# Optimization experiments

Hardware: AMD Instinct MI355X
Metric: run time of the kernel (lower is better)

## Reference

```python
import jax, jax.numpy as jnp
import numpy as np

GRAPH_ALPHA = 3.0
HOP_ALPHA = 0.05
TOP_K = 30


def conv1x1(x, W, b):
    # x: [B,C,N,T], W: [O,C] -> [B,O,N,T]
    return jnp.einsum('bcnt,oc->bont', x, W) + b[None, :, None, None]


def tconv(x, W, b):
    # temporal conv along T, kernel (1,3), 'same' padding. W: [O,I,1,3]
    y = jax.lax.conv_general_dilated(x, W, (1, 1), ((0, 0), (1, 1)),
                                     dimension_numbers=('NCHW', 'OIHW', 'NCHW'))
    return y + b[None, :, None, None]


def mixprop(x, adj, W, b):
    # 1-hop mix-prop graph diffusion (gcn_depth=1, hopalpha=0.05)
    n = adj.shape[0]
    A = adj + jnp.eye(n, dtype=adj.dtype)
    A = A / A.sum(axis=1, keepdims=True)
    h = HOP_ALPHA * x + (1.0 - HOP_ALPHA) * jnp.einsum('bcvt,vw->bcwt', x, A)
    return conv1x1(jnp.concatenate([x, h], axis=1), W, b)


def st_block(x, adj, tf_w, tf_b, tg_w, tg_b, g1_w, g1_b, g2_w, g2_b,
             end_w, end_b, out_w, out_b):
    h = jnp.tanh(tconv(x, tf_w, tf_b)) * jax.nn.sigmoid(tconv(x, tg_w, tg_b))
    h = mixprop(h, adj, g1_w, g1_b) + mixprop(h, adj.T, g2_w, g2_b)
    h = jax.nn.relu(conv1x1(h, end_w, end_b))
    return conv1x1(h, out_w, out_b)


def build_adj(idx, emb1, emb2, l1_w, l1_b, l2_w, l2_b):
    e1, e2 = emb1[idx], emb2[idx]
    n1 = jnp.tanh(GRAPH_ALPHA * (e1 @ l1_w.T + l1_b))
    n2 = jnp.tanh(GRAPH_ALPHA * (e2 @ l2_w.T + l2_b))
    a = n1 @ n2.T - n2 @ n1.T
    adj = jax.nn.relu(jnp.tanh(GRAPH_ALPHA * a))
    _, top_idx = jax.lax.top_k(adj, TOP_K)
    rows = jnp.arange(adj.shape[0])[:, None]
    mask = jnp.zeros_like(adj).at[rows, top_idx].set(1.0)
    return adj * mask


def setup_inputs() -> dict:
    B, T, N, D = 16, 128, 1024, 64
    ks = jax.random.split(jax.random.key(0), 24)
    def w(i, shape):
        return jax.random.normal(ks[i], shape, dtype=jnp.float32) * 0.1
    z = lambda *s: jnp.zeros(s, jnp.float32)
    return {
        'x': jax.random.normal(ks[0], (B, T, N), dtype=jnp.float32),
        'idx': jnp.arange(N, dtype=jnp.int32),
        'emb1': w(1, (N, D)), 'emb2': w(2, (N, D)),
        'lin1_w': w(3, (D, D)), 'lin1_b': z(D),
        'lin2_w': w(4, (D, D)), 'lin2_b': z(D),
        'w_start': w(5, (16, 1)), 'b_start': z(16),
        'enc_tf_w': w(6, (16, 16, 1, 3)), 'enc_tf_b': z(16),
        'enc_tg_w': w(7, (16, 16, 1, 3)), 'enc_tg_b': z(16),
        'enc_g1_w': w(8, (16, 32)), 'enc_g1_b': z(16),
        'enc_g2_w': w(9, (16, 32)), 'enc_g2_b': z(16),
        'enc_end_w': w(10, (32, 16)), 'enc_end_b': z(32),
        'enc_out_w': w(11, (64, 32)), 'enc_out_b': z(64),
        'dec_tf_w': w(12, (64, 64, 1, 3)), 'dec_tf_b': z(64),
        'dec_tg_w': w(13, (64, 64, 1, 3)), 'dec_tg_b': z(64),
        'dec_g1_w': w(14, (64, 128)), 'dec_g1_b': z(64),
        'dec_g2_w': w(15, (64, 128)), 'dec_g2_b': z(64),
        'dec_end_w': w(16, (32, 64)), 'dec_end_b': z(32),
        'dec_out_w': w(17, (16, 32)), 'dec_out_b': z(16),
        'w_end': w(18, (1, 16)), 'b_end': z(1),
    }


def reference(x, idx, emb1, emb2, lin1_w, lin1_b, lin2_w, lin2_b,
              w_start, b_start,
              enc_tf_w, enc_tf_b, enc_tg_w, enc_tg_b, enc_g1_w, enc_g1_b,
              enc_g2_w, enc_g2_b, enc_end_w, enc_end_b, enc_out_w, enc_out_b,
              dec_tf_w, dec_tf_b, dec_tg_w, dec_tg_b, dec_g1_w, dec_g1_b,
              dec_g2_w, dec_g2_b, dec_end_w, dec_end_b, dec_out_w, dec_out_b,
              w_end, b_end):
    adj = build_adj(idx, emb1, emb2, lin1_w, lin1_b, lin2_w, lin2_b)
    h = jnp.transpose(x, (0, 2, 1))[:, None]  # [B,1,N,T]
    h = conv1x1(h, w_start, b_start)          # [B,16,N,T]
    z = st_block(h, adj, enc_tf_w, enc_tf_b, enc_tg_w, enc_tg_b,
                 enc_g1_w, enc_g1_b, enc_g2_w, enc_g2_b,
                 enc_end_w, enc_end_b, enc_out_w, enc_out_b)  # [B,64,N,T]
    y = st_block(z, adj, dec_tf_w, dec_tf_b, dec_tg_w, dec_tg_b,
                 dec_g1_w, dec_g1_b, dec_g2_w, dec_g2_b,
                 dec_end_w, dec_end_b, dec_out_w, dec_out_b)  # [B,16,N,T]
    y = conv1x1(y, w_end, b_end)               # [B,1,N,T]
    return jnp.transpose(y[:, 0], (0, 2, 1))   # [B,T,N]
```

## Files before the change

### kernel.cpp

```cpp
#include <hip/hip_runtime.h>
#include <math.h>

#define NN   1024
#define TTL  128
#define NTP  131072
#define TOPK 30

#define OEGTF_T 0
#define OEGTF_C 48
#define OEGTF_B 96
#define OEGTG_T 112
#define OEGTG_C 160
#define OEGTG_B 208
#define OEE0    224
#define OEE1    736
#define OEE2    1248
#define OEEB    1760
#define OEOUT_W 1792
#define OEOUT_B 3840
#define ODTF_B  16192
#define ODTG_B  28544
#define ODEB    34752
#define OWC     34784
#define OBC     34816
#define ODEALL  59456
#define ODTW2   65600
#define OCF     77888
#define OCG     78080
#define WTOT    78272


__global__ void k_prep_weights(
    const float* __restrict__ w_start, const float* __restrict__ b_start,
    const float* __restrict__ etf_w, const float* __restrict__ etf_b,
    const float* __restrict__ etg_w, const float* __restrict__ etg_b,
    const float* __restrict__ eg1_w, const float* __restrict__ eg1_b,
    const float* __restrict__ eg2_w, const float* __restrict__ eg2_b,
    const float* __restrict__ eend_w, const float* __restrict__ eend_b,
    const float* __restrict__ eout_w, const float* __restrict__ eout_b,
    const float* __restrict__ dtf_w, const float* __restrict__ dtf_b,
    const float* __restrict__ dtg_w, const float* __restrict__ dtg_b,
    const float* __restrict__ dg1_w, const float* __restrict__ dg1_b,
    const float* __restrict__ dg2_w, const float* __restrict__ dg2_b,
    const float* __restrict__ dend_w, const float* __restrict__ dend_b,
    const float* __restrict__ dout_w, const float* __restrict__ dout_b,
    const float* __restrict__ w_end, const float* __restrict__ b_end,
    float* __restrict__ W)
{
    int tid = blockIdx.x*blockDim.x + threadIdx.x;
    int nthr = gridDim.x*blockDim.x;
    for (int id=tid; id<96; id+=nthr){
        int which = id/48; int r = id%48; int o = r/3, k = r%3;
        const float* w = which ? etg_w : etf_w;
        double t=0.0, c=0.0;
        for (int i=0;i<16;i++){
            double wv = (double)w[(o*16+i)*3+k];
            t += wv*(double)w_start[i];
            c += wv*(double)b_start[i];
        }
        W[(which?OEGTG_T:OEGTF_T)+o*3+k] = (float)t;
        W[(which?OEGTG_C:OEGTF_C)+o*3+k] = (float)c;
    }
    for (int i=tid;i<16;i+=nthr){
        W[OEGTF_B+i] = etf_b[i];
        W[OEGTG_B+i] = etg_b[i];
    }
    for (int id=tid; id<512; id+=nthr){
        int i = id>>5, o2 = id&31;
        double s0=0.0, s1=0.0, s2=0.0;
        for (int o=0;o<16;o++){
            double m0 = (double)eg1_w[o*32+i] + (double)eg2_w[o*32+i]
                      + 0.05*((double)eg1_w[o*32+16+i] + (double)eg2_w[o*32+16+i]);
            double m1 = 0.95*(double)eg1_w[o*32+16+i];
            double m2 = 0.95*(double)eg2_w[o*32+16+i];
            double ew = (double)eend_w[o2*16+o];
            s0 += ew*m0; s1 += ew*m1; s2 += ew*m2;
        }
        W[OEE0+i*32+o2]=(float)s0; W[OEE1+i*32+o2]=(float)s1; W[OEE2+i*32+o2]=(float)s2;
    }
    for (int o2=tid; o2<32; o2+=nthr){
        double s = (double)eend_b[o2];
        for (int o=0;o<16;o++) s += (double)eend_w[o2*16+o]*((double)eg1_b[o]+(double)eg2_b[o]);
        W[OEEB+o2] = (float)s;
    }
    for (int i=tid;i<64;i+=nthr){
        W[ODTF_B+i]=dtf_b[i]; W[ODTG_B+i]=dtg_b[i];
    }
    for (int id=tid; id<12288; id+=nthr){
        int oc = id/3072; int rem = id%3072; int j = rem/96; int q = rem%96;
        const float* w = (q<48) ? dtf_w : dtg_w;
        int q2 = (q<48) ? q : q-48;
        int o = q2/3, k = q2%3;
        double s = 0.0;
        for (int i=0;i<64;i++)
            s += (double)w[((oc*16+o)*64+i)*3+k]*(double)eout_w[i*32+j];
        W[ODTW2+id] = (float)s;
    }
    for (int id=tid; id<384; id+=nthr){
        int which = id/192; int r = id%192;
        int oc = r/48; int q = r%48; int o = q/3, k = q%3;
        const float* w = which ? dtg_w : dtf_w;
        double s = 0.0;
        for (int i=0;i<64;i++)
            s += (double)w[((oc*16+o)*64+i)*3+k]*(double)eout_b[i];
        W[(which?OCG:OCF) + oc*48 + o*3 + k] = (float)s;
    }
    for (int id=tid; id<6144; id+=nthr){
        int i = id/96, j = id%96;
        double s = 0.0;
        if (j < 32){
            int o2 = j;
            for (int o=0;o<64;o++){
                double m1 = 0.95*(double)dg1_w[o*128+64+i];
                s += (double)dend_w[o2*64+o]*m1;
            }
        } else if (j < 64){
            int o2 = j-32;
            for (int o=0;o<64;o++){
                double m2 = 0.95*(double)dg2_w[o*128+64+i];
                s += (double)dend_w[o2*64+o]*m2;
            }
        } else {
            int o2 = j-64;
            for (int o=0;o<64;o++){
                double m0 = (double)dg1_w[o*128+i] + (double)dg2_w[o*128+i]
                          + 0.05*((double)dg1_w[o*128+64+i] + (double)dg2_w[o*128+64+i]);
                s += (double)dend_w[o2*64+o]*m0;
            }
        }
        W[ODEALL+id] = (float)s;
    }
    for (int o2=tid; o2<32; o2+=nthr){
        double s = (double)dend_b[o2];
        for (int o=0;o<64;o++) s += (double)dend_w[o2*64+o]*((double)dg1_b[o]+(double)dg2_b[o]);
        W[ODEB+o2] = (float)s;
        double wc = 0.0;
        for (int o3=0;o3<16;o3++) wc += (double)w_end[o3]*(double)dout_w[o3*32+o2];
        W[OWC+o2] = (float)wc;
    }
    if (tid==0){
        double bc = (double)b_end[0];
        for (int o3=0;o3<16;o3++) bc += (double)w_end[o3]*(double)dout_b[o3];
        W[OBC] = (float)bc;
    }
}

__global__ void k_emb(const int* __restrict__ idxp,
                      const float* __restrict__ emb1, const float* __restrict__ emb2,
                      const float* __restrict__ l1w, const float* __restrict__ l1b,
                      const float* __restrict__ l2w, const float* __restrict__ l2b,
                      double* __restrict__ n1, double* __restrict__ n2)
{
    int id = blockIdx.x*blockDim.x + threadIdx.x;
    int i = id>>6, d = id&63;
    int ii = idxp[i];
    double a1 = (double)l1b[d], a2 = (double)l2b[d];
    for (int k=0;k<64;k++){
        a1 += (double)emb1[ii*64+k]*(double)l1w[d*64+k];
        a2 += (double)emb2[ii*64+k]*(double)l2w[d*64+k];
    }
    n1[id] = tanh(3.0*a1);
    n2[id] = tanh(3.0*a2);
}

__global__ __launch_bounds__(64) void k_topk(
    const double* __restrict__ n1, const double* __restrict__ n2,
    int* __restrict__ topc, double* __restrict__ topv,
    double* __restrict__ rs1, double* __restrict__ colsum)
{
    __shared__ double arow[NN];
    __shared__ double sn1[64], sn2[64];
    int i = blockIdx.x, lane = threadIdx.x;
    sn1[lane] = n1[i*64+lane];
    sn2[lane] = n2[i*64+lane];
    __syncthreads();
    for (int jb=0;jb<16;jb++){
        int j = jb*64 + lane;
        const double* p2 = n2 + j*64;
        const double* p1 = n1 + j*64;
        double d1v=0.0, d2v=0.0;
        for (int d=0;d<64;d++){ d1v += sn1[d]*p2[d]; d2v += sn2[d]*p1[d]; }
        double a = tanh(3.0*(d1v - d2v));
        arow[j] = a>0.0 ? a : 0.0;
    }
    __syncthreads();
    double rsum = 0.0;
    for (int r=0;r<TOPK;r++){
        double bv = -2.0; int bj = 1<<30;
        for (int jb=0;jb<16;jb++){
            int j = jb*64+lane;
            double v = arow[j];
            if (v>bv || (v==bv && j<bj)){ bv=v; bj=j; }
        }
        for (int off=32; off>=1; off>>=1){
            double ov = __shfl_xor(bv, off, 64);
            int    oj = __shfl_xor(bj, off, 64);
            if (ov>bv || (ov==bv && oj<bj)){ bv=ov; bj=oj; }
        }
        if (lane == (bj & 63)) arow[bj] = -2.0;
        if (lane == 0){
            topc[i*TOPK+r] = bj;
            topv[i*TOPK+r] = bv;
            if (bv > 0.0) atomicAdd(&colsum[bj], bv);
        }
        rsum += (bv > 0.0 ? bv : 0.0);
        __syncthreads();
    }
    if (lane == 0) rs1[i] = 1.0 + rsum;
}

__global__ void k_csc(const int* __restrict__ topc, const double* __restrict__ topv,
                      const double* __restrict__ rs1,
                      int* __restrict__ ccount, int* __restrict__ cidx, float* __restrict__ cw)
{
    int w = blockIdx.x*blockDim.x + threadIdx.x;
    if (w >= NN) return;
    double rv = rs1[w];
    for (int r=0;r<TOPK;r++){
        double v = topv[w*TOPK+r];
        if (v > 0.0){
            int col = topc[w*TOPK+r];
            int pos = atomicAdd(&ccount[col], 1);
            cidx[(long)col*NN+pos] = w;
            cw  [(long)col*NN+pos] = (float)(v / rv);
        }
    }
}

__global__ void k_pad(int* __restrict__ ccount, int* __restrict__ cidx, float* __restrict__ cw)
{
    int col = blockIdx.x*blockDim.x + threadIdx.x;
    if (col >= NN) return;
    int cnt = ccount[col];
    int padded = (cnt + 7) & ~7;
    for (int e = cnt; e < padded; e++){
        cidx[(long)col*NN + e] = 0;
        cw  [(long)col*NN + e] = 0.0f;
    }
    ccount[col] = padded;
}

__global__ void k_post1(const double* __restrict__ colsum, const double* __restrict__ rs1,
                        double* __restrict__ rs2, float* __restrict__ d1, float* __restrict__ d2)
{
    int v = blockIdx.x*blockDim.x + threadIdx.x;
    if (v >= NN) return;
    double r2 = 1.0 + colsum[v];
    rs2[v] = r2;
    d2[v] = (float)(1.0/r2);
    d1[v] = (float)(1.0/rs1[v]);
}

__global__ void k_post2(const int* __restrict__ topc, const double* __restrict__ topv,
                        const double* __restrict__ rs2, float* __restrict__ ew2)
{
    int e = blockIdx.x*blockDim.x + threadIdx.x;
    if (e >= NN*TOPK) return;
    double v = topv[e];
    ew2[e] = (v > 0.0) ? (float)(v / rs2[topc[e]]) : 0.0f;
}

__global__ __launch_bounds__(256) void k_xT(const float* __restrict__ x, float* __restrict__ xT)
{
    __shared__ float tile[32][33];
    int b = blockIdx.z, t0 = blockIdx.x*32, n0 = blockIdx.y*32;
    int tx = threadIdx.x, ty = threadIdx.y;
    const float* xb = x + (long)b*NTP;
    for (int r=0;r<4;r++){
        int tl = ty + 8*r;
        tile[tl][tx] = xb[(long)(t0+tl)*NN + n0 + tx];
    }
    __syncthreads();
    float* ob = xT + (long)b*NTP;
    for (int r=0;r<4;r++){
        int nl = ty + 8*r;
        ob[(long)(n0+nl)*TTL + t0 + tx] = tile[tx][nl];
    }
}


__global__ __launch_bounds__(256) void k_enc_gg(const float* __restrict__ xT,
    float* __restrict__ eg, float* __restrict__ es1, float* __restrict__ es2,
    const float* __restrict__ Wt,
    const int* __restrict__ ccount, const int* __restrict__ cidx, const float* __restrict__ cw,
    const int* __restrict__ topc, const float* __restrict__ ew2,
    const float* __restrict__ d1, const float* __restrict__ d2,
    long S, int b0)
{
    __shared__ float ldsg[NN*6];
    int tid = threadIdx.x, c = blockIdx.y, cb = blockIdx.z, t0 = blockIdx.x*4;
    float ft[3], fc[3], gt[3], gcc[3];
    #pragma unroll
    for (int k=0;k<3;k++){
        ft[k]=Wt[OEGTF_T+c*3+k]; fc[k]=Wt[OEGTF_C+c*3+k];
        gt[k]=Wt[OEGTG_T+c*3+k]; gcc[k]=Wt[OEGTG_C+c*3+k];
    }
    float fb = Wt[OEGTF_B+c], gb = Wt[OEGTG_B+c];
    const float* xb = xT + (long)(b0+cb)*NTP;
    long base = (long)c*S + (long)cb*NTP;
    for (int k=0;k<16;k++){
        int idx = k*256 + tid;
        int v = idx>>2, tl = idx&3, t = t0+tl;
        const float* xp = xb + (long)v*TTL + t;
        float xc = xp[0];
        float atf = fb + ft[1]*xc + fc[1];
        float atg = gb + gt[1]*xc + gcc[1];
        if (t>0){ float xl = xp[-1]; atf += ft[0]*xl + fc[0]; atg += gt[0]*xl + gcc[0]; }
        if (t<TTL-1){ float xr = xp[1]; atf += ft[2]*xr + fc[2]; atg += gt[2]*xr + gcc[2]; }
        float gv = tanhf(atf)/(1.0f+expf(-atg));
        ldsg[v*6+tl] = gv;
        eg[base + (long)v*TTL + t] = gv;
    }
    __syncthreads();
    for (int wb=0;wb<4;wb++){
        int w = wb*256 + tid;
        const float* gw = &ldsg[w*6];
        float g0=gw[0], g1=gw[1], g2=gw[2], g3=gw[3];
        long p = base + (long)w*TTL + t0;
        float dv = d1[w];
        float a0=g0*dv, a1=g1*dv, a2=g2*dv, a3=g3*dv;
        int cnt = ccount[w];
        const int* ci = cidx + (long)w*NN;
        const float* cv = cw + (long)w*NN;
        for (int e0=0; e0<cnt; e0+=8){
            #pragma unroll
            for (int k=0;k<8;k++){
                float wt_ = cv[e0+k];
                const float* s = &ldsg[ci[e0+k]*6];
                a0 += wt_*s[0]; a1 += wt_*s[1]; a2 += wt_*s[2]; a3 += wt_*s[3];
            }
        }
        es1[p]=a0; es1[p+1]=a1; es1[p+2]=a2; es1[p+3]=a3;
        float d2v = d2[w];
        a0=g0*d2v; a1=g1*d2v; a2=g2*d2v; a3=g3*d2v;
        const int* tc = topc + w*TOPK;
        const float* e2 = ew2 + w*TOPK;
        for (int r0=0;r0<TOPK;r0+=6){
            #pragma unroll
            for (int k=0;k<6;k++){
                float wv = e2[r0+k];
                const float* s = &ldsg[tc[r0+k]*6];
                a0 += wv*s[0]; a1 += wv*s[1]; a2 += wv*s[2]; a3 += wv*s[3];
            }
        }
        es2[p]=a0; es2[p+1]=a1; es2[p+2]=a2; es2[p+3]=a3;
    }
}

__global__ __launch_bounds__(256) void k_enc_tail(const float* __restrict__ Bp,
    float* __restrict__ E32, const float* __restrict__ Wt, long S)
{
    long p = (long)blockIdx.x*256 + threadIdx.x;
    float e[32];
    #pragma unroll
    for (int o2=0;o2<32;o2++) e[o2] = Wt[OEEB+o2];
    for (int i=0;i<16;i++){
        float a = Bp[(long)i*S+p], b = Bp[(long)(16+i)*S+p], c = Bp[(long)(32+i)*S+p];
        const float* w0 = Wt+OEE0+i*32;
        const float* w1 = Wt+OEE1+i*32;
        const float* w2 = Wt+OEE2+i*32;
        #pragma unroll
        for (int o2=0;o2<32;o2++) e[o2] += w0[o2]*a + w1[o2]*b + w2[o2]*c;
    }
    #pragma unroll
    for (int o2=0;o2<32;o2++){
        float v = e[o2];
        E32[(long)o2*S+p] = v>0.0f ? v : 0.0f;
    }
}

__global__ __launch_bounds__(256) void k_dec_gate(const float* __restrict__ E32,
    float* __restrict__ g, const float* __restrict__ Wt, long S)
{
    int bx = blockIdx.x;
    int oc = (bx >> 3) & 3;
    long vpair = (long)(bx >> 5)*8 + (bx & 7);
    int tid = threadIdx.x;
    int t = tid & 127, vv = tid >> 7;
    long vstrip = vpair*2 + vv;
    long pos = vstrip*TTL + t;
    bool hasL = (t>0), hasR = (t<TTL-1);
    float af[16], ag[16];
    #pragma unroll
    for (int o=0;o<16;o++){
        float bf = Wt[ODTF_B+oc*16+o] + Wt[OCF+oc*48+o*3+1];
        float bg = Wt[ODTG_B+oc*16+o] + Wt[OCG+oc*48+o*3+1];
        if (hasL){ bf += Wt[OCF+oc*48+o*3];   bg += Wt[OCG+oc*48+o*3]; }
        if (hasR){ bf += Wt[OCF+oc*48+o*3+2]; bg += Wt[OCG+oc*48+o*3+2]; }
        af[o]=bf; ag[o]=bg;
    }
    #pragma unroll 1
    for (int j=0;j<32;j++){
        const float* xp = E32 + (long)j*S + pos;
        float xc = xp[0];
        float xl = hasL ? xp[-1] : 0.0f;
        float xr = hasR ? xp[1]  : 0.0f;
        const float* wfg = Wt + ODTW2 + (long)(oc*32+j)*96;
        #pragma unroll
        for (int o=0;o<16;o++){
            af[o] += wfg[o*3]*xl + wfg[o*3+1]*xc + wfg[o*3+2]*xr;
            ag[o] += wfg[48+o*3]*xl + wfg[48+o*3+1]*xc + wfg[48+o*3+2]*xr;
        }
    }
    #pragma unroll
    for (int o=0;o<16;o++){
        g[(long)(oc*16+o)*S + pos] = tanhf(af[o])/(1.0f+expf(-ag[o]));
    }
}

__global__ __launch_bounds__(256) void k_dec_conv(const float* __restrict__ g,
    float* __restrict__ Cp, float* __restrict__ P0p,
    const float* __restrict__ Wt, long S)
{
    long p = (long)blockIdx.x*256 + threadIdx.x;
    int jc = blockIdx.y;
    if (jc == 0){
        float a1[32], a2[32];
        #pragma unroll
        for (int jj=0;jj<32;jj++){ a1[jj]=0.0f; a2[jj]=0.0f; }
        #pragma unroll 1
        for (int i=0;i<64;i++){
            float gv = g[(long)i*S+p];
            const float* wr = Wt + ODEALL + i*96;
            #pragma unroll
            for (int jj=0;jj<32;jj++){ a1[jj] += wr[jj]*gv; a2[jj] += wr[32+jj]*gv; }
        }
        #pragma unroll
        for (int jj=0;jj<32;jj++){
            Cp[(long)jj*S+p] = a1[jj];
            Cp[(long)(32+jj)*S+p] = a2[jj];
        }
    } else {
        float a0[32];
        #pragma unroll
        for (int jj=0;jj<32;jj++) a0[jj] = Wt[ODEB+jj];
        #pragma unroll 1
        for (int i=0;i<64;i++){
            float gv = g[(long)i*S+p];
            const float* wr = Wt + ODEALL + i*96 + 64;
            #pragma unroll
            for (int jj=0;jj<32;jj++) a0[jj] += wr[jj]*gv;
        }
        #pragma unroll
        for (int jj=0;jj<32;jj++) P0p[(long)jj*S+p] = a0[jj];
    }
}

__global__ __launch_bounds__(256) void k_graph32(const float* __restrict__ P1,
    const float* __restrict__ P2, float* __restrict__ Q12,
    const int* __restrict__ ccount, const int* __restrict__ cidx, const float* __restrict__ cw,
    const int* __restrict__ topc, const float* __restrict__ ew2,
    const float* __restrict__ d1, const float* __restrict__ d2, long S)
{
    __shared__ float lds[NN*6];
    int tid = threadIdx.x;
    int ch = blockIdx.y;
    int cb = blockIdx.z;
    long base = (long)ch*S + (long)cb*NTP;
    int t0 = blockIdx.x*4;
    float r0[4], r1[4], r2[4], r3[4];
    {
        const float* src = P1 + base;
        for (int k=0;k<16;k++){
            int idx = k*256 + tid;
            int v = idx>>2, tl = idx&3;
            lds[v*6+tl] = src[(long)v*TTL + t0 + tl];
        }
        __syncthreads();
        for (int wb=0;wb<4;wb++){
            int w = wb*256 + tid;
            const float* gw = &lds[w*6];
            float dv = d1[w];
            float a0=gw[0]*dv, a1=gw[1]*dv, a2=gw[2]*dv, a3=gw[3]*dv;
            int cnt = ccount[w];
            const int* ci = cidx + (long)w*NN;
            const float* cv = cw + (long)w*NN;
            for (int e0=0; e0<cnt; e0+=8){
                #pragma unroll
                for (int k=0;k<8;k++){
                    float wt_ = cv[e0+k];
                    const float* s = &lds[ci[e0+k]*6];
                    a0 += wt_*s[0]; a1 += wt_*s[1]; a2 += wt_*s[2]; a3 += wt_*s[3];
                }
            }
            r0[wb]=a0; r1[wb]=a1; r2[wb]=a2; r3[wb]=a3;
        }
    }
    __syncthreads();
    {
        const float* src = P2 + base;
        for (int k=0;k<16;k++){
            int idx = k*256 + tid;
            int v = idx>>2, tl = idx&3;
            lds[v*6+tl] = src[(long)v*TTL + t0 + tl];
        }
        __syncthreads();
        for (int wb=0;wb<4;wb++){
            int w = wb*256 + tid;
            const float* gw = &lds[w*6];
            float dv = d2[w];
            float a0=gw[0]*dv, a1=gw[1]*dv, a2=gw[2]*dv, a3=gw[3]*dv;
            const int* tc = topc + w*TOPK;
            const float* e2 = ew2 + w*TOPK;
            for (int q0=0;q0<TOPK;q0+=6){
                #pragma unroll
                for (int k=0;k<6;k++){
                    float wv = e2[q0+k];
                    const float* s = &lds[tc[q0+k]*6];
                    a0 += wv*s[0]; a1 += wv*s[1]; a2 += wv*s[2]; a3 += wv*s[3];
                }
            }
            long p = base + (long)w*TTL + t0;
            Q12[p]   = r0[wb] + a0;
            Q12[p+1] = r1[wb] + a1;
            Q12[p+2] = r2[wb] + a2;
            Q12[p+3] = r3[wb] + a3;
        }
    }
}

__global__ __launch_bounds__(256) void k_dec_tail(const float* __restrict__ P0,
    const float* __restrict__ Q12,
    const float* __restrict__ Wt, float* __restrict__ out, long S, int b0)
{
    long p = (long)blockIdx.x*256 + threadIdx.x;
    float res = Wt[OBC];
    #pragma unroll 8
    for (int o2=0;o2<32;o2++){
        float e = P0[(long)o2*S+p] + Q12[(long)o2*S+p];
        e = e>0.0f ? e : 0.0f;
        res += Wt[OWC+o2]*e;
    }
    int cb = (int)(p >> 17);
    long r = p & (NTP-1);
    int v = (int)(r >> 7), t = (int)(r & (TTL-1));
    out[((long)(b0+cb)*TTL + t)*NN + v] = res;
}


extern "C" void kernel_launch(void* const* d_in, const int* in_sizes, int n_in,
                              void* d_out, int out_size, void* d_ws, size_t ws_size,
                              hipStream_t stream)
{
    const float* x      = (const float*)d_in[0];
    const int*   idx    = (const int*)  d_in[1];
    const float* emb1   = (const float*)d_in[2];
    const float* emb2   = (const float*)d_in[3];
    const float* lin1_w = (const float*)d_in[4];
    const float* lin1_b = (const float*)d_in[5];
    const float* lin2_w = (const float*)d_in[6];
    const float* lin2_b = (const float*)d_in[7];
    const float* w_start= (const float*)d_in[8];
    const float* b_start= (const float*)d_in[9];
    const float* etf_w  = (const float*)d_in[10];
    const float* etf_b  = (const float*)d_in[11];
    const float* etg_w  = (const float*)d_in[12];
    const float* etg_b  = (const float*)d_in[13];
    const float* eg1_w  = (const float*)d_in[14];
    const float* eg1_b  = (const float*)d_in[15];
    const float* eg2_w  = (const float*)d_in[16];
    const float* eg2_b  = (const float*)d_in[17];
    const float* eend_w = (const float*)d_in[18];
    const float* eend_b = (const float*)d_in[19];
    const float* eout_w = (const float*)d_in[20];
    const float* eout_b = (const float*)d_in[21];
    const float* dtf_w  = (const float*)d_in[22];
    const float* dtf_b  = (const float*)d_in[23];
    const float* dtg_w  = (const float*)d_in[24];
    const float* dtg_b  = (const float*)d_in[25];
    const float* dg1_w  = (const float*)d_in[26];
    const float* dg1_b  = (const float*)d_in[27];
    const float* dg2_w  = (const float*)d_in[28];
    const float* dg2_b  = (const float*)d_in[29];
    const float* dend_w = (const float*)d_in[30];
    const float* dend_b = (const float*)d_in[31];
    const float* dout_w = (const float*)d_in[32];
    const float* dout_b = (const float*)d_in[33];
    const float* w_end  = (const float*)d_in[34];
    const float* b_end  = (const float*)d_in[35];
    float* out = (float*)d_out;

    char* basep = (char*)d_ws;
    size_t cur = 0;
    auto alloc = [&](size_t bytes)->void* {
        void* p = basep + cur;
        cur = (cur + bytes + 511) & ~(size_t)511;
        return p;
    };
    float*  W     = (float*) alloc(WTOT*sizeof(float));
    double* n1    = (double*)alloc(65536*sizeof(double));
    double* n2    = (double*)alloc(65536*sizeof(double));
    double* topv  = (double*)alloc((size_t)NN*TOPK*sizeof(double));
    int*    topc  = (int*)   alloc((size_t)NN*TOPK*sizeof(int));
    double* rs1   = (double*)alloc(NN*sizeof(double));
    double* rs2   = (double*)alloc(NN*sizeof(double));
    double* colsum= (double*)alloc(NN*sizeof(double));
    float*  d1a   = (float*) alloc(NN*sizeof(float));
    float*  d2a   = (float*) alloc(NN*sizeof(float));
    float*  ew2   = (float*) alloc((size_t)NN*TOPK*sizeof(float));
    int*    ccount= (int*)   alloc(NN*sizeof(int));
    int*    cidx  = (int*)   alloc((size_t)NN*NN*sizeof(int));
    float*  cw    = (float*) alloc((size_t)NN*NN*sizeof(float));
    float*  xT    = (float*) alloc((size_t)16*NTP*sizeof(float));

    size_t perb = (size_t)176 * NTP * sizeof(float);
    int CB = 1;
    for (int c = 16; c >= 1; c >>= 1){
        if (cur + perb*(size_t)c <= ws_size){ CB = c; break; }
    }
    long S = (long)CB * NTP;
    float* A = (float*)alloc((size_t)64*S*sizeof(float));
    float* B = (float*)alloc((size_t)48*S*sizeof(float));
    float* C = (float*)alloc((size_t)64*S*sizeof(float));

    (void)hipMemsetAsync(colsum, 0, NN*sizeof(double), stream);
    (void)hipMemsetAsync(ccount, 0, NN*sizeof(int), stream);

    k_prep_weights<<<32,256,0,stream>>>(
        w_start,b_start, etf_w,etf_b, etg_w,etg_b, eg1_w,eg1_b, eg2_w,eg2_b,
        eend_w,eend_b, eout_w,eout_b, dtf_w,dtf_b, dtg_w,dtg_b, dg1_w,dg1_b,
        dg2_w,dg2_b, dend_w,dend_b, dout_w,dout_b, w_end,b_end, W);
    k_emb<<<256,256,0,stream>>>(idx, emb1, emb2, lin1_w, lin1_b, lin2_w, lin2_b, n1, n2);
    k_topk<<<NN,64,0,stream>>>(n1, n2, topc, topv, rs1, colsum);
    k_csc<<<4,256,0,stream>>>(topc, topv, rs1, ccount, cidx, cw);
    k_pad<<<4,256,0,stream>>>(ccount, cidx, cw);
    k_post1<<<4,256,0,stream>>>(colsum, rs1, rs2, d1a, d2a);
    k_post2<<<(NN*TOPK+255)/256,256,0,stream>>>(topc, topv, rs2, ew2);
    k_xT<<<dim3(4,32,16),dim3(32,8),0,stream>>>(x, xT);

    int nch = 16 / CB;
    for (int ch=0; ch<nch; ch++){
        int b0 = ch*CB;
        k_enc_gg<<<dim3(32,16,CB),256,0,stream>>>(xT, B, B+(long)16*S, B+(long)32*S, W,
            ccount,cidx,cw, topc,ew2, d1a,d2a, S, b0);
        k_enc_tail<<<512*CB,256,0,stream>>>(B, A, W, S);
        k_dec_gate<<<2048*CB,256,0,stream>>>(A, C, W, S);
        k_dec_conv<<<dim3(512*CB,2),256,0,stream>>>(C, A, B, W, S);
        k_graph32<<<dim3(32,32,CB),256,0,stream>>>(A, A+(long)32*S, C,
            ccount,cidx,cw, topc,ew2, d1a,d2a, S);
        k_dec_tail<<<512*CB,256,0,stream>>>(B, C, W, out, S, b0);
    }
    (void)in_sizes; (void)n_in; (void)out_size;
}
```

Before: 4.369 ms.

## Switch intermediates to time-major layout and vectorize graph gathers with float4

Intermediate activations now use a [t][node] layout that matches the input x and the output. This removes the separate x transpose kernel and the transposed output store, and makes the graph kernels' LDS staging and global writes coalesced per node. Graph gathers now read packed float4 tiles and fetch CSC indices and weights as int4/float4. The top-k lists are padded to 32 entries so the second-hop loop can be fully vectorized. The decoder gate kernel's temporal neighbours are now NN elements apart, which changes its access pattern and grid shape.

```diff
diff --git a/kernel.cpp b/kernel.cpp
--- a/kernel.cpp
+++ b/kernel.cpp
@@ -252,42 +252,33 @@
 }
 
 __global__ void k_post2(const int* __restrict__ topc, const double* __restrict__ topv,
-                        const double* __restrict__ rs2, float* __restrict__ ew2)
+                        const double* __restrict__ rs2,
+                        int* __restrict__ topc2, float* __restrict__ ew2b)
 {
     int e = blockIdx.x*blockDim.x + threadIdx.x;
-    if (e >= NN*TOPK) return;
-    double v = topv[e];
-    ew2[e] = (v > 0.0) ? (float)(v / rs2[topc[e]]) : 0.0f;
-}
-
-__global__ __launch_bounds__(256) void k_xT(const float* __restrict__ x, float* __restrict__ xT)
-{
-    __shared__ float tile[32][33];
-    int b = blockIdx.z, t0 = blockIdx.x*32, n0 = blockIdx.y*32;
-    int tx = threadIdx.x, ty = threadIdx.y;
-    const float* xb = x + (long)b*NTP;
-    for (int r=0;r<4;r++){
-        int tl = ty + 8*r;
-        tile[tl][tx] = xb[(long)(t0+tl)*NN + n0 + tx];
-    }
-    __syncthreads();
-    float* ob = xT + (long)b*NTP;
-    for (int r=0;r<4;r++){
-        int nl = ty + 8*r;
-        ob[(long)(n0+nl)*TTL + t0 + tx] = tile[tx][nl];
-    }
-}
-
-
-__global__ __launch_bounds__(256) void k_enc_gg(const float* __restrict__ xT,
+    if (e >= NN*32) return;
+    int w = e>>5, r = e&31;
+    if (r < TOPK){
+        double v = topv[w*TOPK+r];
+        int c = topc[w*TOPK+r];
+        topc2[e] = (v > 0.0) ? c : 0;
+        ew2b[e]  = (v > 0.0) ? (float)(v / rs2[c]) : 0.0f;
+    } else {
+        topc2[e] = 0;
+        ew2b[e]  = 0.0f;
+    }
+}
+
+
+__global__ __launch_bounds__(256) void k_enc_gg(const float* __restrict__ x,
     float* __restrict__ eg, float* __restrict__ es1, float* __restrict__ es2,
     const float* __restrict__ Wt,
     const int* __restrict__ ccount, const int* __restrict__ cidx, const float* __restrict__ cw,
-    const int* __restrict__ topc, const float* __restrict__ ew2,
+    const int* __restrict__ topc2, const float* __restrict__ ew2b,
     const float* __restrict__ d1, const float* __restrict__ d2,
     long S, int b0)
 {
-    __shared__ float ldsg[NN*6];
+    __shared__ float4 lds4[NN];
     int tid = threadIdx.x, c = blockIdx.y, cb = blockIdx.z, t0 = blockIdx.x*4;
     float ft[3], fc[3], gt[3], gcc[3];
     #pragma unroll
@@ -296,54 +287,77 @@
         gt[k]=Wt[OEGTG_T+c*3+k]; gcc[k]=Wt[OEGTG_C+c*3+k];
     }
     float fb = Wt[OEGTF_B+c], gb = Wt[OEGTG_B+c];
-    const float* xb = xT + (long)(b0+cb)*NTP;
-    long base = (long)c*S + (long)cb*NTP;
-    for (int k=0;k<16;k++){
-        int idx = k*256 + tid;
-        int v = idx>>2, tl = idx&3, t = t0+tl;
-        const float* xp = xb + (long)v*TTL + t;
-        float xc = xp[0];
-        float atf = fb + ft[1]*xc + fc[1];
-        float atg = gb + gt[1]*xc + gcc[1];
-        if (t>0){ float xl = xp[-1]; atf += ft[0]*xl + fc[0]; atg += gt[0]*xl + gcc[0]; }
-        if (t<TTL-1){ float xr = xp[1]; atf += ft[2]*xr + fc[2]; atg += gt[2]*xr + gcc[2]; }
-        float gv = tanhf(atf)/(1.0f+expf(-atg));
-        ldsg[v*6+tl] = gv;
-        eg[base + (long)v*TTL + t] = gv;
+    const float* xb = x + (long)(b0+cb)*NTP + (long)t0*NN;
+    long base = (long)c*S + (long)cb*NTP + (long)t0*NN;
+    bool hl0 = (t0>0), hr3 = (t0+4<TTL);
+    for (int q=0;q<4;q++){
+        int v = q*256 + tid;
+        float xm = hl0 ? xb[v-NN] : 0.0f;
+        float x0 = xb[v], x1 = xb[v+NN], x2 = xb[v+2*NN], x3 = xb[v+3*NN];
+        float xq = hr3 ? xb[v+4*NN] : 0.0f;
+        float g0,g1,g2,g3;
+        {
+            float atf = fb + ft[1]*x0 + fc[1], atg = gb + gt[1]*x0 + gcc[1];
+            if (hl0){ atf += ft[0]*xm + fc[0]; atg += gt[0]*xm + gcc[0]; }
+            atf += ft[2]*x1 + fc[2]; atg += gt[2]*x1 + gcc[2];
+            g0 = tanhf(atf)/(1.0f+expf(-atg));
+        }
+        {
+            float atf = fb + ft[0]*x0 + fc[0] + ft[1]*x1 + fc[1] + ft[2]*x2 + fc[2];
+            float atg = gb + gt[0]*x0 + gcc[0] + gt[1]*x1 + gcc[1] + gt[2]*x2 + gcc[2];
+            g1 = tanhf(atf)/(1.0f+expf(-atg));
+        }
+        {
+            float atf = fb + ft[0]*x1 + fc[0] + ft[1]*x2 + fc[1] + ft[2]*x3 + fc[2];
+            float atg = gb + gt[0]*x1 + gcc[0] + gt[1]*x2 + gcc[1] + gt[2]*x3 + gcc[2];
+            g2 = tanhf(atf)/(1.0f+expf(-atg));
+        }
+        {
+            float atf = fb + ft[0]*x2 + fc[0] + ft[1]*x3 + fc[1];
+            float atg = gb + gt[0]*x2 + gcc[0] + gt[1]*x3 + gcc[1];
+            if (hr3){ atf += ft[2]*xq + fc[2]; atg += gt[2]*xq + gcc[2]; }
+            g3 = tanhf(atf)/(1.0f+expf(-atg));
+        }
+        lds4[v] = make_float4(g0,g1,g2,g3);
+        eg[base+v] = g0; eg[base+NN+v] = g1; eg[base+2*NN+v] = g2; eg[base+3*NN+v] = g3;
     }
     __syncthreads();
     for (int wb=0;wb<4;wb++){
         int w = wb*256 + tid;
-        const float* gw = &ldsg[w*6];
-        float g0=gw[0], g1=gw[1], g2=gw[2], g3=gw[3];
-        long p = base + (long)w*TTL + t0;
+        float4 gw = lds4[w];
         float dv = d1[w];
-        float a0=g0*dv, a1=g1*dv, a2=g2*dv, a3=g3*dv;
+        float a0=gw.x*dv, a1=gw.y*dv, a2=gw.z*dv, a3=gw.w*dv;
         int cnt = ccount[w];
-        const int* ci = cidx + (long)w*NN;
-        const float* cv = cw + (long)w*NN;
-        for (int e0=0; e0<cnt; e0+=8){
-            #pragma unroll
-            for (int k=0;k<8;k++){
-                float wt_ = cv[e0+k];
-                const float* s = &ldsg[ci[e0+k]*6];
-                a0 += wt_*s[0]; a1 += wt_*s[1]; a2 += wt_*s[2]; a3 += wt_*s[3];
-            }
-        }
-        es1[p]=a0; es1[p+1]=a1; es1[p+2]=a2; es1[p+3]=a3;
-        float d2v = d2[w];
-        a0=g0*d2v; a1=g1*d2v; a2=g2*d2v; a3=g3*d2v;
-        const int* tc = topc + w*TOPK;
-        const float* e2 = ew2 + w*TOPK;
-        for (int r0=0;r0<TOPK;r0+=6){
-            #pragma unroll
-            for (int k=0;k<6;k++){
-                float wv = e2[r0+k];
-                const float* s = &ldsg[tc[r0+k]*6];
-                a0 += wv*s[0]; a1 += wv*s[1]; a2 += wv*s[2]; a3 += wv*s[3];
-            }
-        }
-        es2[p]=a0; es2[p+1]=a1; es2[p+2]=a2; es2[p+3]=a3;
+        const int4*   ci4 = (const int4*)  (cidx + (long)w*NN);
+        const float4* cw4 = (const float4*)(cw   + (long)w*NN);
+        for (int e=0; e<cnt; e+=8){
+            int4 ia = ci4[e>>2], ib = ci4[(e>>2)+1];
+            float4 wa = cw4[e>>2], wc = cw4[(e>>2)+1];
+            float4 s;
+            s = lds4[ia.x]; a0 += wa.x*s.x; a1 += wa.x*s.y; a2 += wa.x*s.z; a3 += wa.x*s.w;
+            s = lds4[ia.y]; a0 += wa.y*s.x; a1 += wa.y*s.y; a2 += wa.y*s.z; a3 += wa.y*s.w;
+            s = lds4[ia.z]; a0 += wa.z*s.x; a1 += wa.z*s.y; a2 += wa.z*s.z; a3 += wa.z*s.w;
+            s = lds4[ia.w]; a0 += wa.w*s.x; a1 += wa.w*s.y; a2 += wa.w*s.z; a3 += wa.w*s.w;
+            s = lds4[ib.x]; a0 += wc.x*s.x; a1 += wc.x*s.y; a2 += wc.x*s.z; a3 += wc.x*s.w;
+            s = lds4[ib.y]; a0 += wc.y*s.x; a1 += wc.y*s.y; a2 += wc.y*s.z; a3 += wc.y*s.w;
+            s = lds4[ib.z]; a0 += wc.z*s.x; a1 += wc.z*s.y; a2 += wc.z*s.z; a3 += wc.z*s.w;
+            s = lds4[ib.w]; a0 += wc.w*s.x; a1 += wc.w*s.y; a2 += wc.w*s.z; a3 += wc.w*s.w;
+        }
+        es1[base+w]=a0; es1[base+NN+w]=a1; es1[base+2*NN+w]=a2; es1[base+3*NN+w]=a3;
+        float dw = d2[w];
+        float b0a=gw.x*dw, b1a=gw.y*dw, b2a=gw.z*dw, b3a=gw.w*dw;
+        const int4*   tc4 = (const int4*)  (topc2 + w*32);
+        const float4* e24 = (const float4*)(ew2b  + w*32);
+        #pragma unroll
+        for (int r=0;r<8;r++){
+            int4 ic = tc4[r]; float4 wv = e24[r];
+            float4 s;
+            s = lds4[ic.x]; b0a += wv.x*s.x; b1a += wv.x*s.y; b2a += wv.x*s.z; b3a += wv.x*s.w;
+            s = lds4[ic.y]; b0a += wv.y*s.x; b1a += wv.y*s.y; b2a += wv.y*s.z; b3a += wv.y*s.w;
+            s = lds4[ic.z]; b0a += wv.z*s.x; b1a += wv.z*s.y; b2a += wv.z*s.z; b3a += wv.z*s.w;
+            s = lds4[ic.w]; b0a += wv.w*s.x; b1a += wv.w*s.y; b2a += wv.w*s.z; b3a += wv.w*s.w;
+        }
+        es2[base+w]=b0a; es2[base+NN+w]=b1a; es2[base+2*NN+w]=b2a; es2[base+3*NN+w]=b3a;
     }
 }
 
@@ -372,13 +386,9 @@
 __global__ __launch_bounds__(256) void k_dec_gate(const float* __restrict__ E32,
     float* __restrict__ g, const float* __restrict__ Wt, long S)
 {
-    int bx = blockIdx.x;
-    int oc = (bx >> 3) & 3;
-    long vpair = (long)(bx >> 5)*8 + (bx & 7);
-    int tid = threadIdx.x;
-    int t = tid & 127, vv = tid >> 7;
-    long vstrip = vpair*2 + vv;
-    long pos = vstrip*TTL + t;
+    int oc = blockIdx.y;
+    long pos = (long)blockIdx.x*256 + threadIdx.x;
+    int t = (int)((pos>>10) & (TTL-1));
     bool hasL = (t>0), hasR = (t<TTL-1);
     float af[16], ag[16];
     #pragma unroll
@@ -393,8 +403,8 @@
     for (int j=0;j<32;j++){
         const float* xp = E32 + (long)j*S + pos;
         float xc = xp[0];
-        float xl = hasL ? xp[-1] : 0.0f;
-        float xr = hasR ? xp[1]  : 0.0f;
+        float xl = hasL ? xp[-NN] : 0.0f;
+        float xr = hasR ? xp[NN]  : 0.0f;
         const float* wfg = Wt + ODTW2 + (long)(oc*32+j)*96;
         #pragma unroll
         for (int o=0;o<16;o++){
@@ -449,73 +459,60 @@
 __global__ __launch_bounds__(256) void k_graph32(const float* __restrict__ P1,
     const float* __restrict__ P2, float* __restrict__ Q12,
     const int* __restrict__ ccount, const int* __restrict__ cidx, const float* __restrict__ cw,
-    const int* __restrict__ topc, const float* __restrict__ ew2,
+    const int* __restrict__ topc2, const float* __restrict__ ew2b,
     const float* __restrict__ d1, const float* __restrict__ d2, long S)
 {
-    __shared__ float lds[NN*6];
+    __shared__ float4 lds4[2*NN];
     int tid = threadIdx.x;
-    int ch = blockIdx.y;
-    int cb = blockIdx.z;
-    long base = (long)ch*S + (long)cb*NTP;
-    int t0 = blockIdx.x*4;
-    float r0[4], r1[4], r2[4], r3[4];
-    {
-        const float* src = P1 + base;
-        for (int k=0;k<16;k++){
-            int idx = k*256 + tid;
-            int v = idx>>2, tl = idx&3;
-            lds[v*6+tl] = src[(long)v*TTL + t0 + tl];
-        }
-        __syncthreads();
-        for (int wb=0;wb<4;wb++){
-            int w = wb*256 + tid;
-            const float* gw = &lds[w*6];
-            float dv = d1[w];
-            float a0=gw[0]*dv, a1=gw[1]*dv, a2=gw[2]*dv, a3=gw[3]*dv;
-            int cnt = ccount[w];
-            const int* ci = cidx + (long)w*NN;
-            const float* cv = cw + (long)w*NN;
-            for (int e0=0; e0<cnt; e0+=8){
-                #pragma unroll
-                for (int k=0;k<8;k++){
-                    float wt_ = cv[e0+k];
-                    const float* s = &lds[ci[e0+k]*6];
-                    a0 += wt_*s[0]; a1 += wt_*s[1]; a2 += wt_*s[2]; a3 += wt_*s[3];
-                }
-            }
-            r0[wb]=a0; r1[wb]=a1; r2[wb]=a2; r3[wb]=a3;
-        }
+    int ch = blockIdx.y, cb = blockIdx.z, t0 = blockIdx.x*4;
+    long base = (long)ch*S + (long)cb*NTP + (long)t0*NN;
+    const float* s1 = P1 + base;
+    const float* s2 = P2 + base;
+    for (int q=0;q<4;q++){
+        int v = q*256 + tid;
+        lds4[v]    = make_float4(s1[v], s1[v+NN], s1[v+2*NN], s1[v+3*NN]);
+        lds4[NN+v] = make_float4(s2[v], s2[v+NN], s2[v+2*NN], s2[v+3*NN]);
     }
     __syncthreads();
-    {
-        const float* src = P2 + base;
-        for (int k=0;k<16;k++){
-            int idx = k*256 + tid;
-            int v = idx>>2, tl = idx&3;
-            lds[v*6+tl] = src[(long)v*TTL + t0 + tl];
-        }
-        __syncthreads();
-        for (int wb=0;wb<4;wb++){
-            int w = wb*256 + tid;
-            const float* gw = &lds[w*6];
-            float dv = d2[w];
-            float a0=gw[0]*dv, a1=gw[1]*dv, a2=gw[2]*dv, a3=gw[3]*dv;
-            const int* tc = topc + w*TOPK;
-            const float* e2 = ew2 + w*TOPK;
-            for (int q0=0;q0<TOPK;q0+=6){
-                #pragma unroll
-                for (int k=0;k<6;k++){
-                    float wv = e2[q0+k];
-                    const float* s = &lds[tc[q0+k]*6];
-                    a0 += wv*s[0]; a1 += wv*s[1]; a2 += wv*s[2]; a3 += wv*s[3];
-                }
-            }
-            long p = base + (long)w*TTL + t0;
-            Q12[p]   = r0[wb] + a0;
-            Q12[p+1] = r1[wb] + a1;
-            Q12[p+2] = r2[wb] + a2;
-            Q12[p+3] = r3[wb] + a3;
-        }
+    for (int wb=0;wb<4;wb++){
+        int w = wb*256 + tid;
+        float4 g1v = lds4[w];
+        float dv = d1[w];
+        float a0=g1v.x*dv, a1=g1v.y*dv, a2=g1v.z*dv, a3=g1v.w*dv;
+        int cnt = ccount[w];
+        const int4*   ci4 = (const int4*)  (cidx + (long)w*NN);
+        const float4* cw4 = (const float4*)(cw   + (long)w*NN);
+        for (int e=0; e<cnt; e+=8){
+            int4 ia = ci4[e>>2], ib = ci4[(e>>2)+1];
+            float4 wa = cw4[e>>2], wc = cw4[(e>>2)+1];
+            float4 s;
+            s = lds4[ia.x]; a0 += wa.x*s.x; a1 += wa.x*s.y; a2 += wa.x*s.z; a3 += wa.x*s.w;
+            s = lds4[ia.y]; a0 += wa.y*s.x; a1 += wa.y*s.y; a2 += wa.y*s.z; a3 += wa.y*s.w;
+            s = lds4[ia.z]; a0 += wa.z*s.x; a1 += wa.z*s.y; a2 += wa.z*s.z; a3 += wa.z*s.w;
+            s = lds4[ia.w]; a0 += wa.w*s.x; a1 += wa.w*s.y; a2 += wa.w*s.z; a3 += wa.w*s.w;
+            s = lds4[ib.x]; a0 += wc.x*s.x; a1 += wc.x*s.y; a2 += wc.x*s.z; a3 += wc.x*s.w;
+            s = lds4[ib.y]; a0 += wc.y*s.x; a1 += wc.y*s.y; a2 += wc.y*s.z; a3 += wc.y*s.w;
+            s = lds4[ib.z]; a0 += wc.z*s.x; a1 += wc.z*s.y; a2 += wc.z*s.z; a3 += wc.z*s.w;
+            s = lds4[ib.w]; a0 += wc.w*s.x; a1 += wc.w*s.y; a2 += wc.w*s.z; a3 += wc.w*s.w;
+        }
+        float4 g2v = lds4[NN+w];
+        float dw = d2[w];
+        float c0=g2v.x*dw, c1=g2v.y*dw, c2=g2v.z*dw, c3=g2v.w*dw;
+        const int4*   tc4 = (const int4*)  (topc2 + w*32);
+        const float4* e24 = (const float4*)(ew2b  + w*32);
+        #pragma unroll
+        for (int r=0;r<8;r++){
+            int4 ic = tc4[r]; float4 wv = e24[r];
+            float4 s;
+            s = lds4[NN+ic.x]; c0 += wv.x*s.x; c1 += wv.x*s.y; c2 += wv.x*s.z; c3 += wv.x*s.w;
+            s = lds4[NN+ic.y]; c0 += wv.y*s.x; c1 += wv.y*s.y; c2 += wv.y*s.z; c3 += wv.y*s.w;
+            s = lds4[NN+ic.z]; c0 += wv.z*s.x; c1 += wv.z*s.y; c2 += wv.z*s.z; c3 += wv.z*s.w;
+            s = lds4[NN+ic.w]; c0 += wv.w*s.x; c1 += wv.w*s.y; c2 += wv.w*s.z; c3 += wv.w*s.w;
+        }
+        Q12[base+w]      = a0+c0;
+        Q12[base+NN+w]   = a1+c1;
+        Q12[base+2*NN+w] = a2+c2;
+        Q12[base+3*NN+w] = a3+c3;
     }
 }
 
@@ -531,10 +528,7 @@
         e = e>0.0f ? e : 0.0f;
         res += Wt[OWC+o2]*e;
     }
-    int cb = (int)(p >> 17);
-    long r = p & (NTP-1);
-    int v = (int)(r >> 7), t = (int)(r & (TTL-1));
-    out[((long)(b0+cb)*TTL + t)*NN + v] = res;
+    out[(long)b0*NTP + p] = res;
 }
 
 
@@ -597,11 +591,11 @@
     double* colsum= (double*)alloc(NN*sizeof(double));
     float*  d1a   = (float*) alloc(NN*sizeof(float));
     float*  d2a   = (float*) alloc(NN*sizeof(float));
-    float*  ew2   = (float*) alloc((size_t)NN*TOPK*sizeof(float));
+    int*    topc2 = (int*)   alloc((size_t)NN*32*sizeof(int));
+    float*  ew2b  = (float*) alloc((size_t)NN*32*sizeof(float));
     int*    ccount= (int*)   alloc(NN*sizeof(int));
     int*    cidx  = (int*)   alloc((size_t)NN*NN*sizeof(int));
     float*  cw    = (float*) alloc((size_t)NN*NN*sizeof(float));
-    float*  xT    = (float*) alloc((size_t)16*NTP*sizeof(float));
 
     size_t perb = (size_t)176 * NTP * sizeof(float);
     int CB = 1;
@@ -625,19 +619,18 @@
     k_csc<<<4,256,0,stream>>>(topc, topv, rs1, ccount, cidx, cw);
     k_pad<<<4,256,0,stream>>>(ccount, cidx, cw);
     k_post1<<<4,256,0,stream>>>(colsum, rs1, rs2, d1a, d2a);
-    k_post2<<<(NN*TOPK+255)/256,256,0,stream>>>(topc, topv, rs2, ew2);
-    k_xT<<<dim3(4,32,16),dim3(32,8),0,stream>>>(x, xT);
+    k_post2<<<(NN*32+255)/256,256,0,stream>>>(topc, topv, rs2, topc2, ew2b);
 
     int nch = 16 / CB;
     for (int ch=0; ch<nch; ch++){
         int b0 = ch*CB;
-        k_enc_gg<<<dim3(32,16,CB),256,0,stream>>>(xT, B, B+(long)16*S, B+(long)32*S, W,
-            ccount,cidx,cw, topc,ew2, d1a,d2a, S, b0);
+        k_enc_gg<<<dim3(32,16,CB),256,0,stream>>>(x, B, B+(long)16*S, B+(long)32*S, W,
+            ccount,cidx,cw, topc2,ew2b, d1a,d2a, S, b0);
         k_enc_tail<<<512*CB,256,0,stream>>>(B, A, W, S);
-        k_dec_gate<<<2048*CB,256,0,stream>>>(A, C, W, S);
+        k_dec_gate<<<dim3(512*CB,4),256,0,stream>>>(A, C, W, S);
         k_dec_conv<<<dim3(512*CB,2),256,0,stream>>>(C, A, B, W, S);
         k_graph32<<<dim3(32,32,CB),256,0,stream>>>(A, A+(long)32*S, C,
-            ccount,cidx,cw, topc,ew2, d1a,d2a, S);
+            ccount,cidx,cw, topc2,ew2b, d1a,d2a, S);
         k_dec_tail<<<512*CB,256,0,stream>>>(B, C, W, out, S, b0);
     }
     (void)in_sizes; (void)n_in; (void)out_size;
```

Measured after the change: 3.764 ms. -13.8%, faster.
